# Performance work log

Measured on AMD Instinct MI355X. Metric: run time of the kernel, lower is better.

Reference implementation:

```python
import jax, jax.numpy as jnp
import numpy as np

CAPACITY = 0.5


def setup_inputs() -> dict:
    key = jax.random.key(0)
    ks = jax.random.split(key, 5)
    b, s, d, dff = 4, 4096, 1024, 4096
    x = jax.random.normal(ks[0], (b, s, d), dtype=jnp.float32)
    attention_mask = jnp.ones((b, s), dtype=jnp.int32)
    Wr = jax.random.normal(ks[1], (d, 1), dtype=jnp.float32) * (1.0 / np.sqrt(d))
    br = jnp.zeros((1,), dtype=jnp.float32)
    W1 = jax.random.normal(ks[2], (d, dff), dtype=jnp.float32) * (1.0 / np.sqrt(d))
    b1 = jnp.zeros((dff,), dtype=jnp.float32)
    W2 = jax.random.normal(ks[3], (dff, d), dtype=jnp.float32) * (1.0 / np.sqrt(dff))
    b2 = jnp.zeros((d,), dtype=jnp.float32)
    return {"x": x, "attention_mask": attention_mask, "Wr": Wr, "br": br,
            "W1": W1, "b1": b1, "W2": W2, "b2": b2}


def _block(filtered_x, router_weights, W1, b1, W2, b2):
    # Stand-in MoD block: residual router-weighted GELU MLP.
    h = jax.nn.gelu(jnp.einsum('bkd,df->bkf', filtered_x, W1) + b1)
    out = jnp.einsum('bkf,fd->bkd', h, W2) + b2
    return filtered_x + router_weights * out  # router_weights: [b,k,1]


def reference(x, attention_mask, Wr, br, W1, b1, W2, b2):
    b, s, d = x.shape
    top_k = int(s * CAPACITY)
    router_logits = jnp.einsum('bsd,do->bso', x, Wr) + br        # [b,s,1]
    scores = jax.nn.sigmoid(router_logits[..., 0])               # [b,s]
    token_weights, token_index = jax.lax.top_k(scores, top_k)    # [b,k]
    sort_order = jnp.argsort(token_index, axis=1)                # positions
    sorted_indices = jnp.take_along_axis(token_index, sort_order, axis=1)  # [b,k]
    filtered_x = jnp.take_along_axis(x, sorted_indices[..., None], axis=1)  # [b,k,d]
    tw = jax.nn.softmax(token_weights, axis=1)                   # softmax over k
    router_weights = jnp.take_along_axis(tw, sort_order, axis=1)[..., None]  # [b,k,1]
    block_out = _block(filtered_x, router_weights, W1, b1, W2, b2)
    batch_idx = jnp.arange(b)[:, None]
    hidden_states = x.at[batch_idx, sorted_indices].set(block_out)
    # aux loss: BCE-with-logits, targets = 1 on selected tokens
    targets = jnp.zeros((b, s), dtype=x.dtype).at[batch_idx, sorted_indices].set(1.0)
    l = router_logits[..., 0]
    aux_loss = jnp.mean(jnp.maximum(l, 0.0) - l * targets + jnp.log1p(jnp.exp(-jnp.abs(l))))
    return hidden_states, aux_loss
```

## Files before the change

### kernel.cpp

```cpp
#include <hip/hip_runtime.h>

#define NB 4
#define SEQ 4096
#define DIM 1024
#define DFF 4096
#define KSEL 2048
#define NTOK (NB * SEQ)
#define MR (NB * KSEL)

typedef float f32x4_t __attribute__((ext_vector_type(4)));
typedef unsigned long u64_t;
typedef unsigned long u64x2_t __attribute__((ext_vector_type(2)));

__device__ __forceinline__ unsigned short f2bf(float f) {
  union { float f; unsigned u; } v; v.f = f;
  unsigned r = v.u + 0x7fffu + ((v.u >> 16) & 1u);
  return (unsigned short)(r >> 16);
}

__device__ __forceinline__ unsigned char f2fp8(float f) {
  return (unsigned char)(__builtin_amdgcn_cvt_pk_fp8_f32(f, f, 0, false) & 0xff);
}

__device__ __forceinline__ int kperm(int kb) {
  return ((kb >> 3) & 3) * 32 + (kb >> 5) * 8 + (kb & 7);
}

#define GLD16(g, l) __builtin_amdgcn_global_load_lds( \
    (const __attribute__((address_space(1))) void*)(g), \
    (__attribute__((address_space(3))) void*)(l), 16, 0, 0)

__global__ void router_kernel(const float* __restrict__ x, const float* __restrict__ Wr,
                              const float* __restrict__ br,
                              float* __restrict__ logits, float* __restrict__ scores) {
  int lane = threadIdx.x & 63;
  int wid  = threadIdx.x >> 6;
  int row  = blockIdx.x * 4 + wid;
  const float4* xr = (const float4*)(x + (size_t)row * DIM);
  const float4* w4 = (const float4*)Wr;
  float sum = 0.f;
#pragma unroll
  for (int i = 0; i < 4; ++i) {
    float4 a = xr[lane + i * 64];
    float4 w = w4[lane + i * 64];
    sum += a.x * w.x + a.y * w.y + a.z * w.z + a.w * w.w;
  }
#pragma unroll
  for (int off = 32; off > 0; off >>= 1) sum += __shfl_down(sum, off);
  if (lane == 0) {
    float l = sum + br[0];
    logits[row] = l;
    scores[row] = 1.f / (1.f + expf(-l));
  }
}

__global__ void rank_kernel(const float* __restrict__ scores, int* __restrict__ sel) {
  __shared__ float s_sc[SEQ];
  int batch = blockIdx.x >> 8;
  int chunk = blockIdx.x & 255;
  int t = threadIdx.x;
  const float4* sb4 = (const float4*)(scores + batch * SEQ);
  float4* ls4 = (float4*)s_sc;
#pragma unroll
  for (int i = 0; i < 4; ++i) ls4[t + i * 256] = sb4[t + i * 256];
  __syncthreads();
  int tok = chunk * 16 + (t >> 4);
  int sg  = t & 15;
  float s = s_sc[tok];
  const float4* seg = ls4 + sg * 64;
  int jbase = sg * 256;
  int rank = 0;
#pragma unroll 4
  for (int j4 = 0; j4 < 64; ++j4) {
    float4 v = seg[j4];
    int j = jbase + j4 * 4;
    rank += (v.x > s || (v.x == s && j     < tok)) ? 1 : 0;
    rank += (v.y > s || (v.y == s && j + 1 < tok)) ? 1 : 0;
    rank += (v.z > s || (v.z == s && j + 2 < tok)) ? 1 : 0;
    rank += (v.w > s || (v.w == s && j + 3 < tok)) ? 1 : 0;
  }
#pragma unroll
  for (int off = 8; off > 0; off >>= 1) rank += __shfl_down(rank, off, 16);
  if (sg == 0) sel[batch * SEQ + tok] = (rank < KSEL) ? 1 : 0;
}

__global__ void pack_kernel(const float* __restrict__ scores, const int* __restrict__ sel,
                            int* __restrict__ rows, float* __restrict__ rwv,
                            int* __restrict__ slot) {
  __shared__ float red[16];
  __shared__ int scn[1024];
  int batch = blockIdx.x;
  int t = threadIdx.x;
  const float* sb = scores + batch * SEQ;
  const int* fb = sel + batch * SEQ;
  float sc[4]; int fl[4];
#pragma unroll
  for (int i = 0; i < 4; ++i) { sc[i] = sb[t * 4 + i]; fl[i] = fb[t * 4 + i]; }
  float m = fmaxf(fmaxf(sc[0], sc[1]), fmaxf(sc[2], sc[3]));
#pragma unroll
  for (int off = 32; off > 0; off >>= 1) m = fmaxf(m, __shfl_down(m, off));
  if ((t & 63) == 0) red[t >> 6] = m;
  __syncthreads();
  if (t == 0) { float v = red[0]; for (int i = 1; i < 16; ++i) v = fmaxf(v, red[i]); red[0] = v; }
  __syncthreads();
  m = red[0];
  __syncthreads();
  float ex[4]; float esum = 0.f;
#pragma unroll
  for (int i = 0; i < 4; ++i) { ex[i] = expf(sc[i] - m); if (fl[i]) esum += ex[i]; }
#pragma unroll
  for (int off = 32; off > 0; off >>= 1) esum += __shfl_down(esum, off);
  if ((t & 63) == 0) red[t >> 6] = esum;
  __syncthreads();
  if (t == 0) { float v = 0.f; for (int i = 0; i < 16; ++i) v += red[i]; red[0] = v; }
  __syncthreads();
  float total = red[0];
  int cnt = fl[0] + fl[1] + fl[2] + fl[3];
  scn[t] = cnt;
  __syncthreads();
  for (int off = 1; off < 1024; off <<= 1) {
    int a = scn[t];
    int b = (t >= off) ? scn[t - off] : 0;
    __syncthreads();
    scn[t] = a + b;
    __syncthreads();
  }
  int p = scn[t] - cnt;
#pragma unroll
  for (int i = 0; i < 4; ++i) {
    if (fl[i]) {
      rows[batch * KSEL + p] = t * 4 + i;
      rwv[batch * KSEL + p]  = ex[i] / total;
      slot[batch * SEQ + t * 4 + i] = batch * KSEL + p;
      ++p;
    }
  }
}

__global__ void gather_copy_kernel(const float* __restrict__ x, const int* __restrict__ sel,
                                   const int* __restrict__ slot,
                                   unsigned char* __restrict__ Xc, float* __restrict__ out) {
  int tokg = blockIdx.x;
  const float4* src = (const float4*)(x + (size_t)tokg * DIM);
  int t = threadIdx.x;
  float4 v = src[t];
  if (sel[tokg]) {
    unsigned lo = (unsigned)__builtin_amdgcn_cvt_pk_fp8_f32(v.x, v.y, 0, false);
    unsigned both = (unsigned)__builtin_amdgcn_cvt_pk_fp8_f32(v.z, v.w, (int)lo, true);
    int k = t * 4;
    int pos = (k & ~127) + kperm(k & 127);
    *(unsigned*)(Xc + (size_t)slot[tokg] * DIM + pos) = both;
  } else {
    ((float4*)(out + (size_t)tokg * DIM))[t] = v;
  }
}

__global__ void transpose_cast2(const float* __restrict__ W1, unsigned char* __restrict__ W1t,
                                const float* __restrict__ W2, unsigned char* __restrict__ W2t) {
  __shared__ float tl[32][33];
  int bid = blockIdx.x;
  const float* W; unsigned char* Wt; int R, C, bx, by;
  if (bid < 4096) { W = W1; Wt = W1t; R = DIM; C = DFF; bx = bid & 127; by = bid >> 7; }
  else { bid -= 4096; W = W2; Wt = W2t; R = DFF; C = DIM; bx = bid & 31; by = bid >> 5; }
  int c0 = bx * 32;
  int r0 = by * 32;
  int tx = threadIdx.x, ty = threadIdx.y;
#pragma unroll
  for (int i = 0; i < 4; ++i)
    tl[ty + i * 8][tx] = W[(size_t)(r0 + ty + i * 8) * C + c0 + tx];
  __syncthreads();
  int k = r0 + tx;
  int pos = (k & ~127) + kperm(k & 127);
#pragma unroll
  for (int i = 0; i < 4; ++i)
    Wt[(size_t)(c0 + ty + i * 8) * R + pos] = f2fp8(16.f * tl[tx][ty + i * 8]);
}

template <int EPI>
__global__ __launch_bounds__(256)
void gemm11(const unsigned char* __restrict__ A, const unsigned char* __restrict__ Bt,
            int M, int N, int K,
            const float* __restrict__ bias,
            unsigned char* __restrict__ Hout,
            const float* __restrict__ x,
            const int* __restrict__ rows,
            const float* __restrict__ rwv,
            float* __restrict__ out) {
  __shared__ __align__(16) unsigned char As[128 * 128];
  __shared__ __align__(16) unsigned char Bs[128 * 128];

  const int t = threadIdx.x;
  const int lane = t & 63;
  const int wid = t >> 6;
  const int wm = wid >> 1;
  const int wn = wid & 1;

  const int nwg = gridDim.x;
  const int qq = nwg >> 3;
  const int nid = (blockIdx.x & 7) * qq + (blockIdx.x >> 3);
  const int gx = N / 128;
  const int by = nid / gx;
  const int bx = nid - by * gx;
  const int bm0 = by * 128;
  const int bn0 = bx * 128;

  const size_t ldb = (size_t)K;
  const char* Ab = (const char*)A + (size_t)bm0 * ldb;
  const char* Bb = (const char*)Bt + (size_t)bn0 * ldb;
  char* AsB = (char*)As;
  char* BsB = (char*)Bs;

  const int srow = t >> 3;
  const size_t stage_off = (size_t)srow * ldb + (size_t)((((t & 7) ^ (srow & 7)) * 16));

  const int cbs0 = ((lane >> 4) * 32     ) ^ ((lane & 7) << 4);
  const int cbs1 = ((lane >> 4) * 32 + 16) ^ ((lane & 7) << 4);

  f32x4_t acc[4][4];
  f32x4_t zero = {0.f, 0.f, 0.f, 0.f};
#pragma unroll
  for (int i = 0; i < 4; ++i)
#pragma unroll
    for (int j = 0; j < 4; ++j) acc[i][j] = zero;

  const int NT = K / 128;

  for (int kt = 0; kt < NT; ++kt) {
    const size_t kb = (size_t)kt * 128 + stage_off;
#pragma unroll
    for (int c = 0; c < 4; ++c)
      GLD16(Ab + kb + (size_t)(c * 32) * ldb, AsB + t * 16 + c * 4096);
#pragma unroll
    for (int c = 0; c < 4; ++c)
      GLD16(Bb + kb + (size_t)(c * 32) * ldb, BsB + t * 16 + c * 4096);
    __syncthreads();

    u64_t am[4][4], bq[4][4];
#pragma unroll
    for (int i = 0; i < 4; ++i) {
      const char* ap = AsB + (wm * 64 + i * 16 + (lane & 15)) * 128;
      u64x2_t lo = *(const u64x2_t*)(ap + cbs0);
      u64x2_t hi = *(const u64x2_t*)(ap + cbs1);
      am[i][0] = lo[0]; am[i][1] = lo[1]; am[i][2] = hi[0]; am[i][3] = hi[1];
    }
#pragma unroll
    for (int j = 0; j < 4; ++j) {
      const char* bp = BsB + (wn * 64 + j * 16 + (lane & 15)) * 128;
      u64x2_t lo = *(const u64x2_t*)(bp + cbs0);
      u64x2_t hi = *(const u64x2_t*)(bp + cbs1);
      bq[j][0] = lo[0]; bq[j][1] = lo[1]; bq[j][2] = hi[0]; bq[j][3] = hi[1];
    }
    __builtin_amdgcn_s_setprio(1);
#pragma unroll
    for (int i = 0; i < 4; ++i)
#pragma unroll
      for (int j = 0; j < 4; ++j)
#pragma unroll
        for (int kk = 0; kk < 4; ++kk)
          acc[i][j] = __builtin_amdgcn_mfma_f32_16x16x32_fp8_fp8(
              (long)am[i][kk], (long)bq[j][kk], acc[i][j], 0, 0, 0);
    __builtin_amdgcn_s_setprio(0);
    __syncthreads();
  }

  const int rb = (lane >> 4) * 4;
  const int cc = lane & 15;
#pragma unroll
  for (int i = 0; i < 4; ++i) {
#pragma unroll
    for (int qi = 0; qi < 4; ++qi) {
      int grow = bm0 + wm * 64 + i * 16 + rb + qi;
      if (EPI == 1) {
#pragma unroll
        for (int j = 0; j < 4; ++j) {
          int gcol = bn0 + wn * 64 + j * 16 + cc;
          float v = acc[i][j][qi] * 0.0625f + bias[gcol];
          float cp = 0.7978845608028654f * (v + 0.044715f * v * v * v);
          float g = v / (1.f + __expf(-2.f * cp));
          int pos = (gcol & ~127) + kperm(gcol & 127);
          Hout[(size_t)grow * N + pos] = f2fp8(g);
        }
      } else {
        int batch = grow >> 11;
        int tok = rows[grow];
        float rw = rwv[grow];
        size_t obase = ((size_t)(batch * SEQ + tok)) * DIM;
#pragma unroll
        for (int j = 0; j < 4; ++j) {
          int gcol = bn0 + wn * 64 + j * 16 + cc;
          float v = acc[i][j][qi] * 0.0625f + bias[gcol];
          out[obase + gcol] = x[obase + gcol] + rw * v;
        }
      }
    }
  }
}

__global__ void aux_kernel(const float* __restrict__ logits, const int* __restrict__ sel,
                           float* __restrict__ out, int out_size) {
  __shared__ float red[16];
  int t = threadIdx.x;
  float sum = 0.f;
  for (int i = t; i < NTOK; i += 1024) {
    float l = logits[i];
    float tgt = sel[i] ? 1.f : 0.f;
    sum += fmaxf(l, 0.f) - l * tgt + log1pf(expf(-fabsf(l)));
  }
#pragma unroll
  for (int off = 32; off > 0; off >>= 1) sum += __shfl_down(sum, off);
  if ((t & 63) == 0) red[t >> 6] = sum;
  __syncthreads();
  if (t == 0) {
    float v = 0.f;
    for (int i = 0; i < 16; ++i) v += red[i];
    out[out_size - 1] = v / (float)NTOK;
  }
}

extern "C" void kernel_launch(void* const* d_in, const int* in_sizes, int n_in,
                              void* d_out, int out_size, void* d_ws, size_t ws_size,
                              hipStream_t stream) {
  const float* x  = (const float*)d_in[0];
  const float* Wr = (const float*)d_in[2];
  const float* br = (const float*)d_in[3];
  const float* W1 = (const float*)d_in[4];
  const float* b1 = (const float*)d_in[5];
  const float* W2 = (const float*)d_in[6];
  const float* b2 = (const float*)d_in[7];
  float* out = (float*)d_out;

  char* ws = (char*)d_ws;
  float* logits = (float*)(ws);
  float* scores = (float*)(ws + 65536);
  int*   sel    = (int*)(ws + 131072);
  int*   rows   = (int*)(ws + 196608);
  float* rwv    = (float*)(ws + 229376);
  int*   slot   = (int*)(ws + 262144);
  unsigned char* W1t = (unsigned char*)(ws + 327680);
  unsigned char* W2t = (unsigned char*)(ws + 327680 + 4194304);
  unsigned char* Xc  = (unsigned char*)(ws + 327680 + 2 * 4194304);
  unsigned char* H   = (unsigned char*)(ws + 327680 + 2 * 4194304 + 8388608);

  transpose_cast2<<<8192, dim3(32, 8), 0, stream>>>(W1, W1t, W2, W2t);
  router_kernel<<<NTOK / 4, 256, 0, stream>>>(x, Wr, br, logits, scores);
  rank_kernel<<<NTOK / 16, 256, 0, stream>>>(scores, sel);
  pack_kernel<<<NB, 1024, 0, stream>>>(scores, sel, rows, rwv, slot);
  gather_copy_kernel<<<NTOK, 256, 0, stream>>>(x, sel, slot, Xc, out);
  gemm11<1><<<(MR / 128) * (DFF / 128), 256, 0, stream>>>(
      Xc, W1t, MR, DFF, DIM, b1, H, nullptr, nullptr, nullptr, nullptr);
  gemm11<2><<<(MR / 128) * (DIM / 128), 256, 0, stream>>>(
      H, W2t, MR, DIM, DFF, b2, nullptr, x, rows, rwv, out);
  aux_kernel<<<1, 1024, 0, stream>>>(logits, sel, out, out_size);
}
```

Baseline: 211.6 us.

## Use 16x16x128 scaled FP8 MFMA and merge weight prep with router

Each group of four 16x16x32 FP8 MFMAs in both GEMMs is replaced by one MI355X scaled 16x16x128 f8f6f4 MFMA with unit scales (0x7f exponent). The K-permuted LDS layout is reused as-is, so its ordering has to match what the wider instruction expects per lane. Separately, the weight transpose-cast kernel and the router kernel are merged into one launch, removing a kernel boundary and letting the two independent jobs overlap. The goal is fewer matrix instructions and issue slots in the dominant GEMMs, with the risk that a mismatch in lane data layout gives wrong results.

```diff
diff --git a/kernel.cpp b/kernel.cpp
--- a/kernel.cpp
+++ b/kernel.cpp
@@ -11,12 +11,7 @@
 typedef float f32x4_t __attribute__((ext_vector_type(4)));
 typedef unsigned long u64_t;
 typedef unsigned long u64x2_t __attribute__((ext_vector_type(2)));
-
-__device__ __forceinline__ unsigned short f2bf(float f) {
-  union { float f; unsigned u; } v; v.f = f;
-  unsigned r = v.u + 0x7fffu + ((v.u >> 16) & 1u);
-  return (unsigned short)(r >> 16);
-}
+typedef int i32x8_t __attribute__((ext_vector_type(8)));
 
 __device__ __forceinline__ unsigned char f2fp8(float f) {
   return (unsigned char)(__builtin_amdgcn_cvt_pk_fp8_f32(f, f, 0, false) & 0xff);
@@ -30,27 +25,49 @@
     (const __attribute__((address_space(1))) void*)(g), \
     (__attribute__((address_space(3))) void*)(l), 16, 0, 0)
 
-__global__ void router_kernel(const float* __restrict__ x, const float* __restrict__ Wr,
-                              const float* __restrict__ br,
-                              float* __restrict__ logits, float* __restrict__ scores) {
-  int lane = threadIdx.x & 63;
-  int wid  = threadIdx.x >> 6;
-  int row  = blockIdx.x * 4 + wid;
-  const float4* xr = (const float4*)(x + (size_t)row * DIM);
-  const float4* w4 = (const float4*)Wr;
-  float sum = 0.f;
-#pragma unroll
-  for (int i = 0; i < 4; ++i) {
-    float4 a = xr[lane + i * 64];
-    float4 w = w4[lane + i * 64];
-    sum += a.x * w.x + a.y * w.y + a.z * w.z + a.w * w.w;
-  }
-#pragma unroll
-  for (int off = 32; off > 0; off >>= 1) sum += __shfl_down(sum, off);
-  if (lane == 0) {
-    float l = sum + br[0];
-    logits[row] = l;
-    scores[row] = 1.f / (1.f + expf(-l));
+__global__ void prep_kernel(const float* __restrict__ W1, unsigned char* __restrict__ W1t,
+                            const float* __restrict__ W2, unsigned char* __restrict__ W2t,
+                            const float* __restrict__ x, const float* __restrict__ Wr,
+                            const float* __restrict__ br,
+                            float* __restrict__ logits, float* __restrict__ scores) {
+  __shared__ float tl[32][33];
+  int bid = blockIdx.x;
+  if (bid < 8192) {
+    const float* W; unsigned char* Wt; int R, C, bx, by;
+    if (bid < 4096) { W = W1; Wt = W1t; R = DIM; C = DFF; bx = bid & 127; by = bid >> 7; }
+    else { bid -= 4096; W = W2; Wt = W2t; R = DFF; C = DIM; bx = bid & 31; by = bid >> 5; }
+    int c0 = bx * 32;
+    int r0 = by * 32;
+    int tx = threadIdx.x & 31, ty = threadIdx.x >> 5;
+#pragma unroll
+    for (int i = 0; i < 4; ++i)
+      tl[ty + i * 8][tx] = W[(size_t)(r0 + ty + i * 8) * C + c0 + tx];
+    __syncthreads();
+    int k = r0 + tx;
+    int pos = (k & ~127) + kperm(k & 127);
+#pragma unroll
+    for (int i = 0; i < 4; ++i)
+      Wt[(size_t)(c0 + ty + i * 8) * R + pos] = f2fp8(16.f * tl[tx][ty + i * 8]);
+  } else {
+    int lane = threadIdx.x & 63;
+    int wid  = threadIdx.x >> 6;
+    int row  = (bid - 8192) * 4 + wid;
+    const float4* xr = (const float4*)(x + (size_t)row * DIM);
+    const float4* w4 = (const float4*)Wr;
+    float sum = 0.f;
+#pragma unroll
+    for (int i = 0; i < 4; ++i) {
+      float4 a = xr[lane + i * 64];
+      float4 w = w4[lane + i * 64];
+      sum += a.x * w.x + a.y * w.y + a.z * w.z + a.w * w.w;
+    }
+#pragma unroll
+    for (int off = 32; off > 0; off >>= 1) sum += __shfl_down(sum, off);
+    if (lane == 0) {
+      float l = sum + br[0];
+      logits[row] = l;
+      scores[row] = 1.f / (1.f + expf(-l));
+    }
   }
 }
 
@@ -155,30 +172,9 @@
   }
 }
 
-__global__ void transpose_cast2(const float* __restrict__ W1, unsigned char* __restrict__ W1t,
-                                const float* __restrict__ W2, unsigned char* __restrict__ W2t) {
-  __shared__ float tl[32][33];
-  int bid = blockIdx.x;
-  const float* W; unsigned char* Wt; int R, C, bx, by;
-  if (bid < 4096) { W = W1; Wt = W1t; R = DIM; C = DFF; bx = bid & 127; by = bid >> 7; }
-  else { bid -= 4096; W = W2; Wt = W2t; R = DFF; C = DIM; bx = bid & 31; by = bid >> 5; }
-  int c0 = bx * 32;
-  int r0 = by * 32;
-  int tx = threadIdx.x, ty = threadIdx.y;
-#pragma unroll
-  for (int i = 0; i < 4; ++i)
-    tl[ty + i * 8][tx] = W[(size_t)(r0 + ty + i * 8) * C + c0 + tx];
-  __syncthreads();
-  int k = r0 + tx;
-  int pos = (k & ~127) + kperm(k & 127);
-#pragma unroll
-  for (int i = 0; i < 4; ++i)
-    Wt[(size_t)(c0 + ty + i * 8) * R + pos] = f2fp8(16.f * tl[tx][ty + i * 8]);
-}
-
 template <int EPI>
 __global__ __launch_bounds__(256)
-void gemm11(const unsigned char* __restrict__ A, const unsigned char* __restrict__ Bt,
+void gemm12(const unsigned char* __restrict__ A, const unsigned char* __restrict__ Bt,
             int M, int N, int K,
             const float* __restrict__ bias,
             unsigned char* __restrict__ Hout,
@@ -235,30 +231,31 @@
       GLD16(Bb + kb + (size_t)(c * 32) * ldb, BsB + t * 16 + c * 4096);
     __syncthreads();
 
-    u64_t am[4][4], bq[4][4];
+    i32x8_t am[4], bq[4];
 #pragma unroll
     for (int i = 0; i < 4; ++i) {
       const char* ap = AsB + (wm * 64 + i * 16 + (lane & 15)) * 128;
-      u64x2_t lo = *(const u64x2_t*)(ap + cbs0);
-      u64x2_t hi = *(const u64x2_t*)(ap + cbs1);
-      am[i][0] = lo[0]; am[i][1] = lo[1]; am[i][2] = hi[0]; am[i][3] = hi[1];
+      union { u64x2_t q[2]; i32x8_t v; } u;
+      u.q[0] = *(const u64x2_t*)(ap + cbs0);
+      u.q[1] = *(const u64x2_t*)(ap + cbs1);
+      am[i] = u.v;
     }
 #pragma unroll
     for (int j = 0; j < 4; ++j) {
       const char* bp = BsB + (wn * 64 + j * 16 + (lane & 15)) * 128;
-      u64x2_t lo = *(const u64x2_t*)(bp + cbs0);
-      u64x2_t hi = *(const u64x2_t*)(bp + cbs1);
-      bq[j][0] = lo[0]; bq[j][1] = lo[1]; bq[j][2] = hi[0]; bq[j][3] = hi[1];
+      union { u64x2_t q[2]; i32x8_t v; } u;
+      u.q[0] = *(const u64x2_t*)(bp + cbs0);
+      u.q[1] = *(const u64x2_t*)(bp + cbs1);
+      bq[j] = u.v;
     }
     __builtin_amdgcn_s_setprio(1);
 #pragma unroll
     for (int i = 0; i < 4; ++i)
 #pragma unroll
       for (int j = 0; j < 4; ++j)
-#pragma unroll
-        for (int kk = 0; kk < 4; ++kk)
-          acc[i][j] = __builtin_amdgcn_mfma_f32_16x16x32_fp8_fp8(
-              (long)am[i][kk], (long)bq[j][kk], acc[i][j], 0, 0, 0);
+        acc[i][j] = __builtin_amdgcn_mfma_scale_f32_16x16x128_f8f6f4(
+            am[i], bq[j], acc[i][j], 0, 0,
+            0, 0x7f7f7f7f, 0, 0x7f7f7f7f);
     __builtin_amdgcn_s_setprio(0);
     __syncthreads();
   }
@@ -341,14 +338,13 @@
   unsigned char* Xc  = (unsigned char*)(ws + 327680 + 2 * 4194304);
   unsigned char* H   = (unsigned char*)(ws + 327680 + 2 * 4194304 + 8388608);
 
-  transpose_cast2<<<8192, dim3(32, 8), 0, stream>>>(W1, W1t, W2, W2t);
-  router_kernel<<<NTOK / 4, 256, 0, stream>>>(x, Wr, br, logits, scores);
+  prep_kernel<<<12288, 256, 0, stream>>>(W1, W1t, W2, W2t, x, Wr, br, logits, scores);
   rank_kernel<<<NTOK / 16, 256, 0, stream>>>(scores, sel);
   pack_kernel<<<NB, 1024, 0, stream>>>(scores, sel, rows, rwv, slot);
   gather_copy_kernel<<<NTOK, 256, 0, stream>>>(x, sel, slot, Xc, out);
-  gemm11<1><<<(MR / 128) * (DFF / 128), 256, 0, stream>>>(
+  gemm12<1><<<(MR / 128) * (DFF / 128), 256, 0, stream>>>(
       Xc, W1t, MR, DFF, DIM, b1, H, nullptr, nullptr, nullptr, nullptr);
-  gemm11<2><<<(MR / 128) * (DIM / 128), 256, 0, stream>>>(
+  gemm12<2><<<(MR / 128) * (DIM / 128), 256, 0, stream>>>(
       H, W2t, MR, DIM, DFF, b2, nullptr, x, rows, rwv, out);
   aux_kernel<<<1, 1024, 0, stream>>>(logits, sel, out, out_size);
 }
```

Result: faster. 203.7 us (-3.7%).
